# Kernel optimization log

Measured on AMD Instinct MI355X. Metric: run time of the kernel, lower is better.

Reference implementation:

```python
import jax, jax.numpy as jnp
import numpy as np

M, D, H, E = 4096, 2048, 2048, 8


def q8(t):
    # Emulate fp8 e4m3 quantize->dequantize (DeepGEMM inputs); scale is all-ones in the source.
    return t.astype(jnp.float8_e4m3fn).astype(jnp.float32)


def setup_inputs() -> dict:
    key = jax.random.key(0)
    k1, k2, k3 = jax.random.split(key, 3)
    x = jax.random.normal(k1, (M, D), dtype=jnp.float32)
    gate_w = jax.random.normal(k2, (E, D), dtype=jnp.float32) * (D ** -0.5)
    gate_b = jnp.zeros((E,), dtype=jnp.float32)
    expert_w = jax.random.normal(k3, (E, H, D), dtype=jnp.float32) * (D ** -0.5)
    return {"x": x, "gate_w": gate_w, "gate_b": gate_b, "expert_w": expert_w}


def reference(x, gate_w, gate_b, expert_w):
    # Gating: softmax over experts. [M, E]
    gate_scores = jax.nn.softmax(x @ gate_w.T + gate_b, axis=-1)
    # fp8 quantize-dequantize of activations and expert weights (rhs_scale == 1).
    x_q = q8(x)                      # [M, D]
    w_q = q8(expert_w)               # [E, H, D]
    # Grouped GEMM (every expert applied to every token), bf16 output like deep_gemm.
    y = jnp.einsum("md,ehd->emh", x_q, w_q).astype(jnp.bfloat16)  # [E, M, H]
    # Weighted combine: sum_e gate[m,e] * y[e,m,h]
    out = jnp.einsum("me,emh->mh", gate_scores, y.astype(jnp.float32))  # [M, H]
    return out
```

## Files before the change

### kernel.cpp

```cpp
#include <hip/hip_runtime.h>
#include <hip/hip_bf16.h>

#define MDIM 4096
#define DDIM 2048
#define HDIM 2048
#define EDIM 8

typedef float v4f __attribute__((ext_vector_type(4)));
typedef int   v4i __attribute__((ext_vector_type(4)));
typedef int   v8i __attribute__((ext_vector_type(8)));

__device__ __forceinline__ void gl2lds16(const void* g, void* l) {
  __builtin_amdgcn_global_load_lds(
      (const __attribute__((address_space(1))) void*)g,
      (__attribute__((address_space(3))) void*)l,
      16, 0, 0);
}

__global__ __launch_bounds__(256) void k_gate_xq(
    const float* __restrict__ x, const float* __restrict__ gw,
    const float* __restrict__ gb, float* __restrict__ gate,
    unsigned char* __restrict__ x8)
{
  const int wid  = threadIdx.x >> 6;
  const int lane = threadIdx.x & 63;
  const int m    = blockIdx.x * 4 + wid;

  const float4* xr = (const float4*)(x + (size_t)m * DDIM);
  unsigned int* qr = (unsigned int*)(x8 + (size_t)m * DDIM);

  float part[EDIM];
#pragma unroll
  for (int e = 0; e < EDIM; ++e) part[e] = 0.f;

#pragma unroll
  for (int it = 0; it < DDIM / 4 / 64; ++it) {
    const int idx = it * 64 + lane;
    const float4 xv = xr[idx];
    int pk = __builtin_amdgcn_cvt_pk_fp8_f32(xv.x, xv.y, 0, false);
    pk = __builtin_amdgcn_cvt_pk_fp8_f32(xv.z, xv.w, pk, true);
    qr[idx] = (unsigned int)pk;
#pragma unroll
    for (int e = 0; e < EDIM; ++e) {
      const float4 wv = ((const float4*)(gw + (size_t)e * DDIM))[idx];
      part[e] += xv.x * wv.x + xv.y * wv.y + xv.z * wv.z + xv.w * wv.w;
    }
  }
#pragma unroll
  for (int e = 0; e < EDIM; ++e) {
#pragma unroll
    for (int off = 32; off > 0; off >>= 1)
      part[e] += __shfl_xor(part[e], off);
  }
  float lg[EDIM];
  float s = 0.f;
#pragma unroll
  for (int e = 0; e < EDIM; ++e) lg[e] = part[e] + gb[e];
  float mx = lg[0];
#pragma unroll
  for (int e = 1; e < EDIM; ++e) mx = fmaxf(mx, lg[e]);
#pragma unroll
  for (int e = 0; e < EDIM; ++e) { lg[e] = expf(lg[e] - mx); s += lg[e]; }
  const float inv = 1.f / s;
  if (lane < EDIM) gate[m * EDIM + lane] = lg[lane] * inv;
}

__global__ void k_wq(const float* __restrict__ w, unsigned char* __restrict__ w8)
{
  const long long n4 = (long long)EDIM * HDIM * DDIM / 4;
  const long long stride = (long long)gridDim.x * blockDim.x;
  for (long long i = (long long)blockIdx.x * blockDim.x + threadIdx.x; i < n4;
       i += stride) {
    const float4 v = ((const float4*)w)[i];
    int pk = __builtin_amdgcn_cvt_pk_fp8_f32(v.x, v.y, 0, false);
    pk = __builtin_amdgcn_cvt_pk_fp8_f32(v.z, v.w, pk, true);
    ((unsigned int*)w8)[i] = (unsigned int)pk;
  }
}

__global__ __launch_bounds__(512, 2) void k_moe_gemm(
    const unsigned char* __restrict__ x8,
    const unsigned char* __restrict__ w8,
    const float* __restrict__ gate,
    float* __restrict__ out)
{
  extern __shared__ unsigned char smem[];

  const int tid  = threadIdx.x;
  const int lane = tid & 63;
  const int wid  = tid >> 6;
  const int wm   = wid >> 1;
  const int wn   = wid & 1;

  const int bid   = blockIdx.x;
  const int xcd   = bid & 7;
  const int local = bid >> 3;
  const int tm    = (xcd >> 1) * 4 + (local >> 3);
  const int tn    = (xcd & 1) * 8 + (local & 7);
  const int bm    = tm * 256;
  const int bn    = tn * 128;

  const int lrow = lane & 15;
  const int lk   = lane >> 4;
  const int swz  = (lrow & 7) << 4;
  const int c0   = (lk * 32) ^ swz;
  const int c1   = (lk * 32 + 16) ^ swz;

  float* sG = (float*)(smem + 3 * 49152);

  const int strow = tid >> 3;
  const int stcol = ((tid & 7) * 16) ^ ((strow & 7) << 4);
  const unsigned char* abase[4];
  const unsigned char* bbase[2];
#pragma unroll
  for (int i = 0; i < 4; ++i)
    abase[i] = x8 + (size_t)(bm + i * 64 + strow) * DDIM + stcol;
#pragma unroll
  for (int i = 0; i < 2; ++i)
    bbase[i] = w8 + (size_t)(bn + i * 64 + strow) * DDIM + stcol;

  v4f outacc[4][4];
  v4f acc[4][4];
#pragma unroll
  for (int i = 0; i < 4; ++i)
#pragma unroll
    for (int j = 0; j < 4; ++j) {
      outacc[i][j][0] = 0.f; outacc[i][j][1] = 0.f;
      outacc[i][j][2] = 0.f; outacc[i][j][3] = 0.f;
      acc[i][j][0] = 0.f; acc[i][j][1] = 0.f;
      acc[i][j][2] = 0.f; acc[i][j][3] = 0.f;
    }

#define STAGE(IT, BUF) do {                                                    \
    const int e_ = (IT) >> 4;                                                  \
    const int k_ = ((IT) & 15) * 128;                                          \
    const size_t boff_ = (size_t)e_ * ((size_t)HDIM * DDIM) + k_;              \
    unsigned char* la_ = smem + (BUF) * 49152;                                 \
    unsigned char* lb_ = la_ + 32768;                                          \
    _Pragma("unroll") for (int i = 0; i < 4; ++i)                              \
      gl2lds16(abase[i] + k_, (void*)(la_ + i * 8192 + wid * 1024));           \
    _Pragma("unroll") for (int i = 0; i < 2; ++i)                              \
      gl2lds16(bbase[i] + boff_, (void*)(lb_ + i * 8192 + wid * 1024));        \
  } while (0)

#define COMP(BUF, T) do {                                                      \
    const unsigned char* pA_ = smem + (BUF) * 49152 +                          \
                               (size_t)(wm * 64 + lrow) * 128;                 \
    const unsigned char* pB_ = smem + (BUF) * 49152 + 32768 +                  \
                               (size_t)(wn * 64 + lrow) * 128;                 \
    v8i av_[4];                                                                \
    _Pragma("unroll") for (int f = 0; f < 4; ++f) {                            \
      union { v8i v; v4i h[2]; } u_;                                           \
      u_.h[0] = *(const v4i*)(pA_ + f * 2048 + c0);                            \
      u_.h[1] = *(const v4i*)(pA_ + f * 2048 + c1);                            \
      av_[f] = u_.v;                                                           \
    }                                                                          \
    __builtin_amdgcn_s_setprio(1);                                             \
    _Pragma("unroll") for (int j = 0; j < 4; ++j) {                            \
      union { v8i v; v4i h[2]; } u_;                                           \
      u_.h[0] = *(const v4i*)(pB_ + j * 2048 + c0);                            \
      u_.h[1] = *(const v4i*)(pB_ + j * 2048 + c1);                            \
      const v8i bv_ = u_.v;                                                    \
      _Pragma("unroll") for (int i = 0; i < 4; ++i)                            \
        acc[i][j] = __builtin_amdgcn_mfma_scale_f32_16x16x128_f8f6f4(          \
            av_[i], bv_, acc[i][j], 0 , 0 ,                      \
            0, 127 , 0, 127 );                         \
    }                                                                          \
    __builtin_amdgcn_s_setprio(0);                                             \
    if (((T) & 15) == 15) {                                                    \
      const int e_ = (T) >> 4;                                                 \
      _Pragma("unroll") for (int i = 0; i < 4; ++i)                            \
        _Pragma("unroll") for (int q = 0; q < 4; ++q) {                        \
          const float g_ = sG[(wm * 64 + i * 16 + lk * 4 + q) * 8 + e_];       \
          _Pragma("unroll") for (int j = 0; j < 4; ++j) {                      \
            const float yb_ =                                                  \
                __bfloat162float(__float2bfloat16(acc[i][j][q]));              \
            outacc[i][j][q] += g_ * yb_;                                       \
            acc[i][j][q] = 0.f;                                                \
          }                                                                    \
        }                                                                      \
    }                                                                          \
  } while (0)

#define STEP(T, BUF, SBUF, WAIT) do {                                          \
    if ((T) + 2 < 128) STAGE((T) + 2, (SBUF));                                 \
    asm volatile("s_waitcnt vmcnt(" #WAIT ")" ::: "memory");                   \
    __builtin_amdgcn_s_barrier();                                              \
    __builtin_amdgcn_sched_barrier(0);                                         \
    COMP((BUF), (T));                                                          \
    __builtin_amdgcn_sched_barrier(0);                                         \
    __builtin_amdgcn_s_barrier();                                              \
  } while (0)

  {
    const float4 gv = *(const float4*)(gate + (size_t)bm * EDIM + tid * 4);
    ((float4*)sG)[tid] = gv;
  }
  STAGE(0, 0);
  STAGE(1, 1);
  __syncthreads();

  for (int t0 = 0; t0 < 126; t0 += 3) {
    STEP(t0 + 0, 0, 2, 12);
    STEP(t0 + 1, 1, 0, 12);
    STEP(t0 + 2, 2, 1, 12);
  }
  STEP(126, 0, 2, 6);
  STEP(127, 1, 2, 0);

#undef STEP
#undef COMP
#undef STAGE

#pragma unroll
  for (int i = 0; i < 4; ++i)
#pragma unroll
    for (int q = 0; q < 4; ++q) {
      const size_t r = (size_t)(bm + wm * 64 + i * 16 + lk * 4 + q);
      float* orow = out + r * HDIM + bn + wn * 64 + lrow;
#pragma unroll
      for (int j = 0; j < 4; ++j)
        orow[j * 16] = outacc[i][j][q];
    }
}

extern "C" void kernel_launch(void* const* d_in, const int* in_sizes, int n_in,
                              void* d_out, int out_size, void* d_ws, size_t ws_size,
                              hipStream_t stream) {
  (void)in_sizes; (void)n_in; (void)out_size; (void)ws_size;
  const float* x        = (const float*)d_in[0];
  const float* gate_w   = (const float*)d_in[1];
  const float* gate_b   = (const float*)d_in[2];
  const float* expert_w = (const float*)d_in[3];
  float* out = (float*)d_out;

  char* ws = (char*)d_ws;
  float* gate       = (float*)ws;
  unsigned char* x8 = (unsigned char*)(ws + 131072);
  unsigned char* w8 = (unsigned char*)(ws + 131072 + (size_t)MDIM * DDIM);

  hipLaunchKernelGGL(k_gate_xq, dim3(MDIM / 4), dim3(256), 0, stream,
                     x, gate_w, gate_b, gate, x8);
  hipLaunchKernelGGL(k_wq, dim3(4096), dim3(256), 0, stream, expert_w, w8);
  hipLaunchKernelGGL(k_moe_gemm, dim3(256), dim3(512),
                     3 * 49152 + 8192, stream, x8, w8, gate, out);
}
```

Baseline: 191.3 us.

## Use 4-wave blocks with 128x64 warp tiles and double-buffered LDS

Each block drops from 8 to 4 waves, and each wave now computes a 128x64 output tile (8x4 MFMA fragments) so more A/B fragment reuse happens in registers. Triple-buffered LDS staging becomes a simple double-buffered loop. The gate values are stored transposed in LDS so each wave reads them with one vector load. The bf16 rounding of per-expert partial results before the weighted combine is removed. Register pressure roughly doubles and prefetch depth shrinks, which risks spills and less latency hiding, and dropping the rounding slightly changes numerics relative to the reference.

```diff
diff --git a/kernel.cpp b/kernel.cpp
--- a/kernel.cpp
+++ b/kernel.cpp
@@ -5,6 +5,7 @@
 #define DDIM 2048
 #define HDIM 2048
 #define EDIM 8
+#define HD   ((size_t)HDIM * DDIM)
 
 typedef float v4f __attribute__((ext_vector_type(4)));
 typedef int   v4i __attribute__((ext_vector_type(4)));
@@ -78,7 +79,7 @@
   }
 }
 
-__global__ __launch_bounds__(512, 2) void k_moe_gemm(
+__global__ __launch_bounds__(256, 1) void k_moe_gemm(
     const unsigned char* __restrict__ x8,
     const unsigned char* __restrict__ w8,
     const float* __restrict__ gate,
@@ -102,121 +103,112 @@
 
   const int lrow = lane & 15;
   const int lk   = lane >> 4;
-  const int swz  = (lrow & 7) << 4;
-  const int c0   = (lk * 32) ^ swz;
-  const int c1   = (lk * 32 + 16) ^ swz;
-
-  float* sG = (float*)(smem + 3 * 49152);
+  const int c0   = (lk * 32) ^ ((lrow & 7) << 4);
+  const int c1   = c0 ^ 16;
 
   const int strow = tid >> 3;
   const int stcol = ((tid & 7) * 16) ^ ((strow & 7) << 4);
-  const unsigned char* abase[4];
-  const unsigned char* bbase[2];
-#pragma unroll
-  for (int i = 0; i < 4; ++i)
-    abase[i] = x8 + (size_t)(bm + i * 64 + strow) * DDIM + stcol;
-#pragma unroll
-  for (int i = 0; i < 2; ++i)
-    bbase[i] = w8 + (size_t)(bn + i * 64 + strow) * DDIM + stcol;
-
-  v4f outacc[4][4];
-  v4f acc[4][4];
-#pragma unroll
-  for (int i = 0; i < 4; ++i)
+  const unsigned char* asrc = x8 + (size_t)(bm + strow) * DDIM + stcol;
+  const unsigned char* bsrc = w8 + (size_t)(bn + strow) * DDIM + stcol;
+
+  float* sGf = (float*)(smem + 98304);
+
+  {
+    const float4 g0 = *(const float4*)(gate + (size_t)(bm + tid) * EDIM);
+    const float4 g1 = *(const float4*)(gate + (size_t)(bm + tid) * EDIM + 4);
+    sGf[0 * 256 + tid] = g0.x; sGf[1 * 256 + tid] = g0.y;
+    sGf[2 * 256 + tid] = g0.z; sGf[3 * 256 + tid] = g0.w;
+    sGf[4 * 256 + tid] = g1.x; sGf[5 * 256 + tid] = g1.y;
+    sGf[6 * 256 + tid] = g1.z; sGf[7 * 256 + tid] = g1.w;
+  }
+
+  v4f acc[8][4];
+  v4f outacc[8][4];
+#pragma unroll
+  for (int i = 0; i < 8; ++i)
 #pragma unroll
     for (int j = 0; j < 4; ++j) {
+      acc[i][j][0] = 0.f; acc[i][j][1] = 0.f;
+      acc[i][j][2] = 0.f; acc[i][j][3] = 0.f;
       outacc[i][j][0] = 0.f; outacc[i][j][1] = 0.f;
       outacc[i][j][2] = 0.f; outacc[i][j][3] = 0.f;
-      acc[i][j][0] = 0.f; acc[i][j][1] = 0.f;
-      acc[i][j][2] = 0.f; acc[i][j][3] = 0.f;
     }
 
-#define STAGE(IT, BUF) do {                                                    \
-    const int e_ = (IT) >> 4;                                                  \
-    const int k_ = ((IT) & 15) * 128;                                          \
-    const size_t boff_ = (size_t)e_ * ((size_t)HDIM * DDIM) + k_;              \
-    unsigned char* la_ = smem + (BUF) * 49152;                                 \
-    unsigned char* lb_ = la_ + 32768;                                          \
+#define STAGE(S) do {                                                          \
+    const int    kb_ = ((S) & 15) * 128;                                       \
+    const size_t eo_ = (size_t)((S) >> 4) * HD;                                \
+    unsigned char* la_ = smem + ((S) & 1) * 32768;                             \
+    unsigned char* lb_ = smem + 65536 + ((S) & 1) * 16384;                     \
+    _Pragma("unroll") for (int i = 0; i < 8; ++i)                              \
+      gl2lds16(asrc + (size_t)i * (32 * DDIM) + kb_,                           \
+               (void*)(la_ + i * 4096 + wid * 1024));                          \
     _Pragma("unroll") for (int i = 0; i < 4; ++i)                              \
-      gl2lds16(abase[i] + k_, (void*)(la_ + i * 8192 + wid * 1024));           \
-    _Pragma("unroll") for (int i = 0; i < 2; ++i)                              \
-      gl2lds16(bbase[i] + boff_, (void*)(lb_ + i * 8192 + wid * 1024));        \
+      gl2lds16(bsrc + eo_ + (size_t)i * (32 * DDIM) + kb_,                     \
+               (void*)(lb_ + i * 4096 + wid * 1024));                          \
   } while (0)
 
-#define COMP(BUF, T) do {                                                      \
-    const unsigned char* pA_ = smem + (BUF) * 49152 +                          \
-                               (size_t)(wm * 64 + lrow) * 128;                 \
-    const unsigned char* pB_ = smem + (BUF) * 49152 + 32768 +                  \
+#define COMP(S) do {                                                           \
+    const unsigned char* pA_ = smem + ((S) & 1) * 32768 +                      \
+                               (size_t)(wm * 128 + lrow) * 128;                \
+    const unsigned char* pB_ = smem + 65536 + ((S) & 1) * 16384 +              \
                                (size_t)(wn * 64 + lrow) * 128;                 \
-    v8i av_[4];                                                                \
-    _Pragma("unroll") for (int f = 0; f < 4; ++f) {                            \
-      union { v8i v; v4i h[2]; } u_;                                           \
-      u_.h[0] = *(const v4i*)(pA_ + f * 2048 + c0);                            \
-      u_.h[1] = *(const v4i*)(pA_ + f * 2048 + c1);                            \
-      av_[f] = u_.v;                                                           \
-    }                                                                          \
-    __builtin_amdgcn_s_setprio(1);                                             \
+    v8i bv_[4];                                                                \
     _Pragma("unroll") for (int j = 0; j < 4; ++j) {                            \
       union { v8i v; v4i h[2]; } u_;                                           \
       u_.h[0] = *(const v4i*)(pB_ + j * 2048 + c0);                            \
       u_.h[1] = *(const v4i*)(pB_ + j * 2048 + c1);                            \
-      const v8i bv_ = u_.v;                                                    \
-      _Pragma("unroll") for (int i = 0; i < 4; ++i)                            \
+      bv_[j] = u_.v;                                                           \
+    }                                                                          \
+    __builtin_amdgcn_s_setprio(1);                                             \
+    _Pragma("unroll") for (int i = 0; i < 8; ++i) {                            \
+      union { v8i v; v4i h[2]; } ua_;                                          \
+      ua_.h[0] = *(const v4i*)(pA_ + i * 2048 + c0);                           \
+      ua_.h[1] = *(const v4i*)(pA_ + i * 2048 + c1);                           \
+      const v8i av_ = ua_.v;                                                   \
+      _Pragma("unroll") for (int j = 0; j < 4; ++j)                            \
         acc[i][j] = __builtin_amdgcn_mfma_scale_f32_16x16x128_f8f6f4(          \
-            av_[i], bv_, acc[i][j], 0 , 0 ,                      \
+            av_, bv_[j], acc[i][j], 0 , 0 ,                      \
             0, 127 , 0, 127 );                         \
     }                                                                          \
     __builtin_amdgcn_s_setprio(0);                                             \
-    if (((T) & 15) == 15) {                                                    \
-      const int e_ = (T) >> 4;                                                 \
-      _Pragma("unroll") for (int i = 0; i < 4; ++i)                            \
-        _Pragma("unroll") for (int q = 0; q < 4; ++q) {                        \
-          const float g_ = sG[(wm * 64 + i * 16 + lk * 4 + q) * 8 + e_];       \
-          _Pragma("unroll") for (int j = 0; j < 4; ++j) {                      \
-            const float yb_ =                                                  \
-                __bfloat162float(__float2bfloat16(acc[i][j][q]));              \
-            outacc[i][j][q] += g_ * yb_;                                       \
-            acc[i][j][q] = 0.f;                                                \
-          }                                                                    \
+    if (((S) & 15) == 15) {         \
+      const int e_ = (S) >> 4;                                                 \
+      _Pragma("unroll") for (int i = 0; i < 8; ++i) {                          \
+        const v4f g4_ =                                                        \
+            *(const v4f*)(sGf + e_ * 256 + wm * 128 + i * 16 + lk * 4);        \
+        _Pragma("unroll") for (int j = 0; j < 4; ++j) {                        \
+          outacc[i][j][0] += g4_[0] * acc[i][j][0]; acc[i][j][0] = 0.f;        \
+          outacc[i][j][1] += g4_[1] * acc[i][j][1]; acc[i][j][1] = 0.f;        \
+          outacc[i][j][2] += g4_[2] * acc[i][j][2]; acc[i][j][2] = 0.f;        \
+          outacc[i][j][3] += g4_[3] * acc[i][j][3]; acc[i][j][3] = 0.f;        \
         }                                                                      \
+      }                                                                        \
     }                                                                          \
   } while (0)
 
-#define STEP(T, BUF, SBUF, WAIT) do {                                          \
-    if ((T) + 2 < 128) STAGE((T) + 2, (SBUF));                                 \
-    asm volatile("s_waitcnt vmcnt(" #WAIT ")" ::: "memory");                   \
-    __builtin_amdgcn_s_barrier();                                              \
-    __builtin_amdgcn_sched_barrier(0);                                         \
-    COMP((BUF), (T));                                                          \
-    __builtin_amdgcn_sched_barrier(0);                                         \
-    __builtin_amdgcn_s_barrier();                                              \
-  } while (0)
-
-  {
-    const float4 gv = *(const float4*)(gate + (size_t)bm * EDIM + tid * 4);
-    ((float4*)sG)[tid] = gv;
-  }
-  STAGE(0, 0);
-  STAGE(1, 1);
+  STAGE(0);
   __syncthreads();
 
-  for (int t0 = 0; t0 < 126; t0 += 3) {
-    STEP(t0 + 0, 0, 2, 12);
-    STEP(t0 + 1, 1, 0, 12);
-    STEP(t0 + 2, 2, 1, 12);
-  }
-  STEP(126, 0, 2, 6);
-  STEP(127, 1, 2, 0);
-
-#undef STEP
+  for (int s = 0; s < 127; ++s) {
+    STAGE(s + 1);
+    asm volatile("s_waitcnt vmcnt(12)" ::: "memory");
+    __builtin_amdgcn_s_barrier();
+    __builtin_amdgcn_sched_barrier(0);
+    COMP(s);
+    __builtin_amdgcn_s_barrier();
+  }
+  asm volatile("s_waitcnt vmcnt(0)" ::: "memory");
+  __builtin_amdgcn_s_barrier();
+  COMP(127);
+
 #undef COMP
 #undef STAGE
 
 #pragma unroll
-  for (int i = 0; i < 4; ++i)
+  for (int i = 0; i < 8; ++i)
 #pragma unroll
     for (int q = 0; q < 4; ++q) {
-      const size_t r = (size_t)(bm + wm * 64 + i * 16 + lk * 4 + q);
+      const size_t r = (size_t)(bm + wm * 128 + i * 16 + lk * 4 + q);
       float* orow = out + r * HDIM + bn + wn * 64 + lrow;
 #pragma unroll
       for (int j = 0; j < 4; ++j)
@@ -242,6 +234,6 @@
   hipLaunchKernelGGL(k_gate_xq, dim3(MDIM / 4), dim3(256), 0, stream,
                      x, gate_w, gate_b, gate, x8);
   hipLaunchKernelGGL(k_wq, dim3(4096), dim3(256), 0, stream, expert_w, w8);
-  hipLaunchKernelGGL(k_moe_gemm, dim3(256), dim3(512),
-                     3 * 49152 + 8192, stream, x8, w8, gate, out);
-}
+  hipLaunchKernelGGL(k_moe_gemm, dim3(256), dim3(256), 106496, stream,
+                     x8, w8, gate, out);
+}
```

After: 209.9 us. +9.7%, slower.
